# Optimization experiments

Hardware: AMD Instinct MI355X
Metric: run time of the kernel (lower is better)

The kernel has to match this reference:

```python
import jax, jax.numpy as jnp
import numpy as np

EPS = 1e-12


def _gather_neighbors(t, idx):
    # t: (bs, v, d), idx: (bs, v, n) -> (bs, v, n, d)  [torch: t[arange(bs)[:,None,None], idx]]
    bs, v, n = idx.shape
    flat = jnp.take_along_axis(t, idx.reshape(bs, v * n)[..., None], axis=1)
    return flat.reshape(bs, v, n, t.shape[-1])


def setup_inputs() -> dict:
    key = jax.random.key(0)
    ks = jax.random.split(key, 9)
    bs, v, n, inc, outc, sup = 8, 2048, 20, 64, 128, 2
    return {
        "neighbor_index": jax.random.randint(ks[0], (bs, v, n), 0, v),
        "vertices": jax.random.normal(ks[1], (bs, v, 3), dtype=jnp.float32),
        "feature_map": jax.random.normal(ks[2], (bs, v, inc), dtype=jnp.float32),
        "weights": jax.random.normal(ks[3], (inc, (sup + 1) * outc), dtype=jnp.float32) * 0.05,
        "bias": jax.random.normal(ks[4], ((sup + 1) * outc,), dtype=jnp.float32) * 0.05,
        "directions": jax.random.normal(ks[5], (3, sup * outc), dtype=jnp.float32) * 0.05,
        "distance_w": jax.random.normal(ks[6], (1, sup * outc), dtype=jnp.float32) * 0.05,
        "mlp_w": jax.random.normal(ks[7], (outc, 2 * outc), dtype=jnp.float32) * 0.05,
        "mlp_b": jax.random.normal(ks[8], (outc,), dtype=jnp.float32) * 0.05,
    }


def reference(neighbor_index, vertices, feature_map, weights, bias, directions, distance_w, mlp_w, mlp_b):
    bs, v, n = neighbor_index.shape
    outc = mlp_w.shape[0]
    sup = directions.shape[1] // outc

    # neighbor directions and distances (single gather, reuse norm)
    neighbors = _gather_neighbors(vertices, neighbor_index)          # (bs,v,n,3)
    direction = neighbors - vertices[:, :, None, :]                  # (bs,v,n,3)
    dist = jnp.linalg.norm(direction, axis=-1)                       # (bs,v,n)
    dir_norm = direction / jnp.maximum(dist[..., None], EPS)         # F.normalize
    dist_max = jnp.max(dist, axis=2, keepdims=True)                  # (bs,v,1)

    # support directions normalized along dim 0
    sdn = directions / jnp.maximum(jnp.linalg.norm(directions, axis=0, keepdims=True), EPS)
    theta = jax.nn.relu(jnp.einsum('bvnc,cs->bvns', dir_norm, sdn))  # (bs,v,n,sup*outc)
    dist_feat = jax.nn.relu(dist_max @ distance_w)                   # (bs,v,sup*outc)

    feat = feature_map @ weights + bias                              # (bs,v,(sup+1)*outc)
    center = feat[..., :outc]
    support = feat[..., outc:]
    support_g = _gather_neighbors(support, neighbor_index)           # (bs,v,n,sup*outc)

    act = (theta * support_g).reshape(bs, v, n, sup, outc)
    act = jnp.sum(jnp.max(act, axis=2), axis=2)                      # max over neighbors, sum over supports
    fuse = center + act                                              # (bs,v,outc)
    dist_sum = jnp.sum(dist_feat.reshape(bs, v, sup, outc), axis=2)  # (bs,v,outc)

    out = jnp.concatenate([fuse, dist_sum], axis=-1)                 # (bs,v,2*outc)
    return out @ mlp_w.T + mlp_b                                     # (bs,v,outc)
```

## Files before the change

### kernel.cpp

```cpp
#include <hip/hip_runtime.h>
#include <hip/hip_bf16.h>

#define BS    8
#define V     2048
#define NNB   20
#define INC   64
#define OUTC  128
#define SUP   2
#define NCOL  ((SUP + 1) * OUTC)
#define SCOL  (SUP * OUTC)
#define ROWS  (BS * V)
#define XPAD  136

using bf16x8 = __bf16 __attribute__((ext_vector_type(8)));
using bf16x4 = __bf16 __attribute__((ext_vector_type(4)));
using f32x4  = float  __attribute__((ext_vector_type(4)));
using f32x2  = float  __attribute__((ext_vector_type(2)));
using i32x4  = int    __attribute__((ext_vector_type(4)));
using u16x4  = unsigned short __attribute__((ext_vector_type(4)));

#if __has_builtin(__builtin_elementwise_fma)
static __device__ inline f32x2 efma(f32x2 a, f32x2 b, f32x2 c) { return __builtin_elementwise_fma(a, b, c); }
#else
static __device__ inline f32x2 efma(f32x2 a, f32x2 b, f32x2 c) {
    f32x2 r; r[0] = fmaf(a[0], b[0], c[0]); r[1] = fmaf(a[1], b[1], c[1]); return r;
}
#endif
#if __has_builtin(__builtin_elementwise_max)
static __device__ inline f32x2 emax(f32x2 a, f32x2 b) { return __builtin_elementwise_max(a, b); }
#else
static __device__ inline f32x2 emax(f32x2 a, f32x2 b) {
    f32x2 r; r[0] = fmaxf(a[0], b[0]); r[1] = fmaxf(a[1], b[1]); return r;
}
#endif

static __device__ inline bf16x8 cvt8(f32x4 lo, f32x4 hi) {
    bf16x8 r;
    r[0] = (__bf16)lo[0]; r[1] = (__bf16)lo[1]; r[2] = (__bf16)lo[2]; r[3] = (__bf16)lo[3];
    r[4] = (__bf16)hi[0]; r[5] = (__bf16)hi[1]; r[6] = (__bf16)hi[2]; r[7] = (__bf16)hi[3];
    return r;
}

static __device__ inline float b2f(unsigned short u) {
    union { unsigned int i; float f; } c; c.i = ((unsigned int)u) << 16; return c.f;
}

__global__ __launch_bounds__(256) void k_prep(const float* __restrict__ W,
                                              const float* __restrict__ Wm,
                                              const float* __restrict__ dw,
                                              __bf16* __restrict__ WTb,
                                              __bf16* __restrict__ Wm1b,
                                              float* __restrict__ w2) {
    const int b = blockIdx.x;
    if (b < 96) {
        const int idx = b * 256 + threadIdx.x;
        const int c = idx >> 6, k = idx & 63;
        WTb[idx] = (__bf16)W[k * NCOL + c];
    } else if (b < 160) {
        const int idx = (b - 96) * 256 + threadIdx.x;
        const int o = idx >> 7, k = idx & 127;
        Wm1b[idx] = (__bf16)Wm[o * SCOL + k];
    } else {
        __shared__ float u[OUTC];
        const int t = threadIdx.x;
        if (t < OUTC) u[t] = fmaxf(dw[t], 0.f) + fmaxf(dw[OUTC + t], 0.f);
        __syncthreads();
        if (t < OUTC) {
            float s = 0.f;
            for (int k = 0; k < OUTC; ++k) s = fmaf(Wm[t * SCOL + OUTC + k], u[k], s);
            w2[t] = s;
        }
    }
}

__global__ __launch_bounds__(256) void k_feat(const float* __restrict__ fm,
                                              const __bf16* __restrict__ WTb,
                                              const float* __restrict__ bias,
                                              float* __restrict__ center,
                                              __bf16* __restrict__ supb) {
    const int row0 = blockIdx.x * 32;
    const int wid = threadIdx.x >> 6, lane = threadIdx.x & 63;
    const int ln = lane & 15, lg = lane >> 4;
    const int cbase = wid * 96;

    bf16x8 a[2][2];
#pragma unroll
    for (int rs = 0; rs < 2; ++rs) {
        const float* ap = fm + (size_t)(row0 + rs * 16 + ln) * INC + lg * 8;
        a[rs][0] = cvt8(*(const f32x4*)(ap +  0), *(const f32x4*)(ap +  4));
        a[rs][1] = cvt8(*(const f32x4*)(ap + 32), *(const f32x4*)(ap + 36));
    }

    f32x4 acc[2][6];
#pragma unroll
    for (int t = 0; t < 6; ++t) {
        const float bb = bias[cbase + t * 16 + ln];
        acc[0][t] = (f32x4){bb, bb, bb, bb};
        acc[1][t] = acc[0][t];
    }

    const __bf16* bp = WTb + (size_t)(cbase + ln) * INC + lg * 8;
#pragma unroll
    for (int t = 0; t < 6; ++t) {
        const bf16x8 b0 = *(const bf16x8*)(bp + t * 16 * INC);
        const bf16x8 b1 = *(const bf16x8*)(bp + t * 16 * INC + 32);
        acc[0][t] = __builtin_amdgcn_mfma_f32_16x16x32_bf16(a[0][0], b0, acc[0][t], 0, 0, 0);
        acc[0][t] = __builtin_amdgcn_mfma_f32_16x16x32_bf16(a[0][1], b1, acc[0][t], 0, 0, 0);
        acc[1][t] = __builtin_amdgcn_mfma_f32_16x16x32_bf16(a[1][0], b0, acc[1][t], 0, 0, 0);
        acc[1][t] = __builtin_amdgcn_mfma_f32_16x16x32_bf16(a[1][1], b1, acc[1][t], 0, 0, 0);
    }

#pragma unroll
    for (int rs = 0; rs < 2; ++rs) {
        const int r0 = row0 + rs * 16 + lg * 4;
#pragma unroll
        for (int t = 0; t < 6; ++t) {
            const int col = cbase + t * 16 + ln;
            if (col < OUTC) {
#pragma unroll
                for (int r = 0; r < 4; ++r)
                    center[(size_t)(r0 + r) * OUTC + col] = acc[rs][t][r];
            } else {
                const int sc = col - OUTC;
#pragma unroll
                for (int r = 0; r < 4; ++r)
                    supb[(size_t)(r0 + r) * SCOL + sc] = (__bf16)acc[rs][t][r];
            }
        }
    }
}

__global__ __launch_bounds__(256, 4) void k_no(const int*   __restrict__ nbr,
                                               const float* __restrict__ verts,
                                               const float* __restrict__ dirs,
                                               const float* __restrict__ center,
                                               const __bf16* __restrict__ supb,
                                               const __bf16* __restrict__ Wm1b,
                                               const float* __restrict__ w2,
                                               const float* __restrict__ mb,
                                               float* __restrict__ out) {
    const int bid   = blockIdx.x;
    const int batch = bid & 7;
    const int chunk = bid >> 3;
    const int u0    = chunk * 16;
    const int bV    = batch * V;
    const int tid   = threadIdx.x;
    const int wid   = tid >> 6;
    const int lane  = tid & 63;
    const int half  = lane >> 5;
    const int sl    = lane & 31;
    const int c0    = sl * 4;
    const int ln    = lane & 15, lg = lane >> 4;

    __shared__ __bf16 Xl[16][XPAD];
    __shared__ float  dl[16];

    f32x4 A0 = *(const f32x4*)(dirs +            c0);
    f32x4 A1 = *(const f32x4*)(dirs + SCOL +     c0);
    f32x4 A2 = *(const f32x4*)(dirs + 2*SCOL +   c0);
    f32x4 B0 = *(const f32x4*)(dirs +            OUTC + c0);
    f32x4 B1 = *(const f32x4*)(dirs + SCOL +     OUTC + c0);
    f32x4 B2 = *(const f32x4*)(dirs + 2*SCOL +   OUTC + c0);
#pragma unroll
    for (int j = 0; j < 4; ++j) {
        float inv = __builtin_amdgcn_rsqf(fmaxf(fmaf(A0[j], A0[j], fmaf(A1[j], A1[j], A2[j]*A2[j])), 1e-24f));
        A0[j] *= inv; A1[j] *= inv; A2[j] *= inv;
        inv = __builtin_amdgcn_rsqf(fmaxf(fmaf(B0[j], B0[j], fmaf(B1[j], B1[j], B2[j]*B2[j])), 1e-24f));
        B0[j] *= inv; B1[j] *= inv; B2[j] *= inv;
    }
    const f32x2 ax0 = {A0[0], A0[1]}, ax1 = {A0[2], A0[3]};
    const f32x2 ay0 = {A1[0], A1[1]}, ay1 = {A1[2], A1[3]};
    const f32x2 az0 = {A2[0], A2[1]}, az1 = {A2[2], A2[3]};
    const f32x2 bx0 = {B0[0], B0[1]}, bx1 = {B0[2], B0[3]};
    const f32x2 by0 = {B1[0], B1[1]}, by1 = {B1[2], B1[3]};
    const f32x2 bz0 = {B2[0], B2[1]}, bz1 = {B2[2], B2[3]};
    const f32x2 zero = {0.f, 0.f};

    const __bf16* supBase = supb + (size_t)bV * SCOL + c0;

#pragma unroll
    for (int p = 0; p < 2; ++p) {
        const int ul  = p * 8 + wid * 2 + half;
        const int row = bV + u0 + ul;

        const float vx = verts[row * 3 + 0];
        const float vy = verts[row * 3 + 1];
        const float vz = verts[row * 3 + 2];

        int gs[NNB];
        {
            const i32x4* np4 = reinterpret_cast<const i32x4*>(nbr + (size_t)row * NNB);
#pragma unroll
            for (int t = 0; t < 5; ++t) {
                const i32x4 g4 = np4[t];
                gs[t*4+0] = g4[0]; gs[t*4+1] = g4[1]; gs[t*4+2] = g4[2]; gs[t*4+3] = g4[3];
            }
        }

        f32x2 mA0 = {-INFINITY, -INFINITY}, mA1 = mA0, mB0 = mA0, mB1 = mA0;
        float d2max = 0.f;

#pragma unroll
        for (int t = 0; t < 4; ++t) {
            u16x4 s0r[5], s1r[5];
            float px[5], py[5], pz[5];
#pragma unroll
            for (int q = 0; q < 5; ++q) {
                const int g = gs[t * 5 + q];
                const __bf16* sg = supBase + (size_t)g * SCOL;
                s0r[q] = *(const u16x4*)(sg);
                s1r[q] = *(const u16x4*)(sg + OUTC);
                const float* vp = verts + (size_t)(bV + g) * 3;
                px[q] = vp[0]; py[q] = vp[1]; pz[q] = vp[2];
            }
#pragma unroll
            for (int q = 0; q < 5; ++q) {
                const float dx = px[q] - vx, dy = py[q] - vy, dz = pz[q] - vz;
                const float d2 = fmaf(dx, dx, fmaf(dy, dy, dz * dz));
                d2max = fmaxf(d2max, d2);
                const float inv = __builtin_amdgcn_rsqf(fmaxf(d2, 1e-24f));
                const f32x2 nX = {dx * inv, dx * inv};
                const f32x2 nY = {dy * inv, dy * inv};
                const f32x2 nZ = {dz * inv, dz * inv};

                const f32x2 s0lo = {b2f(s0r[q][0]), b2f(s0r[q][1])};
                const f32x2 s0hi = {b2f(s0r[q][2]), b2f(s0r[q][3])};
                const f32x2 s1lo = {b2f(s1r[q][0]), b2f(s1r[q][1])};
                const f32x2 s1hi = {b2f(s1r[q][2]), b2f(s1r[q][3])};

                const f32x2 tA0 = emax(efma(nZ, az0, efma(nY, ay0, nX * ax0)), zero);
                const f32x2 tA1 = emax(efma(nZ, az1, efma(nY, ay1, nX * ax1)), zero);
                const f32x2 tB0 = emax(efma(nZ, bz0, efma(nY, by0, nX * bx0)), zero);
                const f32x2 tB1 = emax(efma(nZ, bz1, efma(nY, by1, nX * bx1)), zero);
                mA0 = emax(mA0, tA0 * s0lo);
                mA1 = emax(mA1, tA1 * s0hi);
                mB0 = emax(mB0, tB0 * s1lo);
                mB1 = emax(mB1, tB1 * s1hi);
            }
        }

        const f32x4 cc = *(const f32x4*)(center + (size_t)row * OUTC + c0);
        const f32x2 f01 = (f32x2){cc[0], cc[1]} + mA0 + mB0;
        const f32x2 f23 = (f32x2){cc[2], cc[3]} + mA1 + mB1;
        bf16x4 fx;
        fx[0] = (__bf16)f01[0]; fx[1] = (__bf16)f01[1];
        fx[2] = (__bf16)f23[0]; fx[3] = (__bf16)f23[1];
        *(bf16x4*)(&Xl[ul][c0]) = fx;
        if (sl == 0) dl[ul] = sqrtf(d2max);
    }
    __syncthreads();

    {
        const int cb = wid * 32;

        bf16x8 a[4];
#pragma unroll
        for (int kf = 0; kf < 4; ++kf)
            a[kf] = *(const bf16x8*)(&Xl[ln][lg * 8 + kf * 32]);

        f32x4 acc[2];
        acc[0] = (f32x4)0.f; acc[1] = (f32x4)0.f;

        const __bf16* bp = Wm1b + (size_t)(cb + ln) * OUTC + lg * 8;
#pragma unroll
        for (int t = 0; t < 2; ++t) {
#pragma unroll
            for (int kf = 0; kf < 4; ++kf) {
                const bf16x8 b = *(const bf16x8*)(bp + t * 16 * OUTC + kf * 32);
                acc[t] = __builtin_amdgcn_mfma_f32_16x16x32_bf16(a[kf], b, acc[t], 0, 0, 0);
            }
        }

        float dm[4];
#pragma unroll
        for (int r = 0; r < 4; ++r) dm[r] = dl[lg * 4 + r];

        const int rowg0 = bV + u0 + lg * 4;
#pragma unroll
        for (int t = 0; t < 2; ++t) {
            const int col = cb + t * 16 + ln;
            const float w2c = w2[col];
            const float bb  = mb[col];
#pragma unroll
            for (int r = 0; r < 4; ++r)
                out[(size_t)(rowg0 + r) * OUTC + col] = fmaf(dm[r], w2c, acc[t][r] + bb);
        }
    }
}

extern "C" void kernel_launch(void* const* d_in, const int* in_sizes, int n_in,
                              void* d_out, int out_size, void* d_ws, size_t ws_size,
                              hipStream_t stream) {
    const int*   nbr   = (const int*)  d_in[0];
    const float* verts = (const float*)d_in[1];
    const float* fm    = (const float*)d_in[2];
    const float* W     = (const float*)d_in[3];
    const float* bias  = (const float*)d_in[4];
    const float* dirs  = (const float*)d_in[5];
    const float* dw    = (const float*)d_in[6];
    const float* Wm    = (const float*)d_in[7];
    const float* mb    = (const float*)d_in[8];
    float* out = (float*)d_out;

    float*  center  = (float*)d_ws;
    __bf16* supb    = (__bf16*)(center + (size_t)ROWS * OUTC);
    __bf16* WTb     = supb + (size_t)ROWS * SCOL;
    __bf16* Wm1b    = WTb + NCOL * INC;
    float*  w2      = (float*)(Wm1b + OUTC * OUTC);

    k_prep <<<161,        256, 0, stream>>>(W, Wm, dw, WTb, Wm1b, w2);
    k_feat <<<ROWS / 32,  256, 0, stream>>>(fm, WTb, bias, center, supb);
    k_no   <<<ROWS / 16,  256, 0, stream>>>(nbr, verts, dirs, center, supb, Wm1b, w2, mb, out);
}
```

Measured before the change: 117.3 us.

## Interleave vertex coordinates into support rows and halve rows per block

Packs each vertex's xyz into a padded slot at the end of its bf16 support-feature row, so a neighbor gather gets features and coordinates from one contiguous row rather than from two arrays. k_prep gains blocks that write the coordinates, and the gather loop is regrouped as 5x4 instead of 4x5. k_no now handles 8 vertices per block with twice as many blocks and an occupancy hint of 8. The MFMA tail still computes 16 rows, so half of that work is discarded.

```diff
diff --git a/kernel.cpp b/kernel.cpp
--- a/kernel.cpp
+++ b/kernel.cpp
@@ -12,6 +12,10 @@
 #define ROWS  (BS * V)
 #define XPAD  136
 
+#define SROW_B   528
+#define SROW_E   264
+#define XYZ_OFF  512
+
 using bf16x8 = __bf16 __attribute__((ext_vector_type(8)));
 using bf16x4 = __bf16 __attribute__((ext_vector_type(4)));
 using f32x4  = float  __attribute__((ext_vector_type(4)));
@@ -48,9 +52,11 @@
 __global__ __launch_bounds__(256) void k_prep(const float* __restrict__ W,
                                               const float* __restrict__ Wm,
                                               const float* __restrict__ dw,
+                                              const float* __restrict__ verts,
                                               __bf16* __restrict__ WTb,
                                               __bf16* __restrict__ Wm1b,
-                                              float* __restrict__ w2) {
+                                              float* __restrict__ w2,
+                                              __bf16* __restrict__ supx) {
     const int b = blockIdx.x;
     if (b < 96) {
         const int idx = b * 256 + threadIdx.x;
@@ -60,7 +66,7 @@
         const int idx = (b - 96) * 256 + threadIdx.x;
         const int o = idx >> 7, k = idx & 127;
         Wm1b[idx] = (__bf16)Wm[o * SCOL + k];
-    } else {
+    } else if (b == 160) {
         __shared__ float u[OUTC];
         const int t = threadIdx.x;
         if (t < OUTC) u[t] = fmaxf(dw[t], 0.f) + fmaxf(dw[OUTC + t], 0.f);
@@ -70,6 +76,14 @@
             for (int k = 0; k < OUTC; ++k) s = fmaf(Wm[t * SCOL + OUTC + k], u[k], s);
             w2[t] = s;
         }
+    } else {
+        const int idx = (b - 161) * 256 + threadIdx.x;
+        f32x4 wv;
+        wv[0] = verts[(size_t)idx * 3 + 0];
+        wv[1] = verts[(size_t)idx * 3 + 1];
+        wv[2] = verts[(size_t)idx * 3 + 2];
+        wv[3] = 0.f;
+        *(f32x4*)((char*)supx + (size_t)idx * SROW_B + XYZ_OFF) = wv;
     }
 }
 
@@ -77,7 +91,7 @@
                                               const __bf16* __restrict__ WTb,
                                               const float* __restrict__ bias,
                                               float* __restrict__ center,
-                                              __bf16* __restrict__ supb) {
+                                              __bf16* __restrict__ supx) {
     const int row0 = blockIdx.x * 32;
     const int wid = threadIdx.x >> 6, lane = threadIdx.x & 63;
     const int ln = lane & 15, lg = lane >> 4;
@@ -124,17 +138,16 @@
                 const int sc = col - OUTC;
 #pragma unroll
                 for (int r = 0; r < 4; ++r)
-                    supb[(size_t)(r0 + r) * SCOL + sc] = (__bf16)acc[rs][t][r];
-            }
-        }
-    }
-}
-
-__global__ __launch_bounds__(256, 4) void k_no(const int*   __restrict__ nbr,
-                                               const float* __restrict__ verts,
+                    supx[(size_t)(r0 + r) * SROW_E + sc] = (__bf16)acc[rs][t][r];
+            }
+        }
+    }
+}
+
+__global__ __launch_bounds__(256, 8) void k_no(const int*   __restrict__ nbr,
                                                const float* __restrict__ dirs,
                                                const float* __restrict__ center,
-                                               const __bf16* __restrict__ supb,
+                                               const __bf16* __restrict__ supx,
                                                const __bf16* __restrict__ Wm1b,
                                                const float* __restrict__ w2,
                                                const float* __restrict__ mb,
@@ -142,7 +155,7 @@
     const int bid   = blockIdx.x;
     const int batch = bid & 7;
     const int chunk = bid >> 3;
-    const int u0    = chunk * 16;
+    const int u0    = chunk * 8;
     const int bV    = batch * V;
     const int tid   = threadIdx.x;
     const int wid   = tid >> 6;
@@ -176,16 +189,15 @@
     const f32x2 bz0 = {B2[0], B2[1]}, bz1 = {B2[2], B2[3]};
     const f32x2 zero = {0.f, 0.f};
 
-    const __bf16* supBase = supb + (size_t)bV * SCOL + c0;
-
-#pragma unroll
-    for (int p = 0; p < 2; ++p) {
-        const int ul  = p * 8 + wid * 2 + half;
-        const int row = bV + u0 + ul;
-
-        const float vx = verts[row * 3 + 0];
-        const float vy = verts[row * 3 + 1];
-        const float vz = verts[row * 3 + 2];
+    const char* supB = (const char*)supx + (size_t)bV * SROW_B;
+
+    {
+        const int ul  = wid * 2 + half;
+        const int u   = u0 + ul;
+        const int row = bV + u;
+
+        const f32x4 self = *(const f32x4*)(supB + (size_t)u * SROW_B + XYZ_OFF);
+        const float vx = self[0], vy = self[1], vz = self[2];
 
         int gs[NNB];
         {
@@ -201,21 +213,19 @@
         float d2max = 0.f;
 
 #pragma unroll
-        for (int t = 0; t < 4; ++t) {
-            u16x4 s0r[5], s1r[5];
-            float px[5], py[5], pz[5];
-#pragma unroll
-            for (int q = 0; q < 5; ++q) {
-                const int g = gs[t * 5 + q];
-                const __bf16* sg = supBase + (size_t)g * SCOL;
-                s0r[q] = *(const u16x4*)(sg);
-                s1r[q] = *(const u16x4*)(sg + OUTC);
-                const float* vp = verts + (size_t)(bV + g) * 3;
-                px[q] = vp[0]; py[q] = vp[1]; pz[q] = vp[2];
-            }
-#pragma unroll
-            for (int q = 0; q < 5; ++q) {
-                const float dx = px[q] - vx, dy = py[q] - vy, dz = pz[q] - vz;
+        for (int t = 0; t < 5; ++t) {
+            u16x4 s0r[4], s1r[4];
+            f32x4 nxyz[4];
+#pragma unroll
+            for (int q = 0; q < 4; ++q) {
+                const char* nb = supB + (size_t)gs[t * 4 + q] * SROW_B + (size_t)(sl * 8);
+                s0r[q]  = *(const u16x4*)(nb);
+                s1r[q]  = *(const u16x4*)(nb + 256);
+                nxyz[q] = *(const f32x4*)(supB + (size_t)gs[t * 4 + q] * SROW_B + XYZ_OFF);
+            }
+#pragma unroll
+            for (int q = 0; q < 4; ++q) {
+                const float dx = nxyz[q][0] - vx, dy = nxyz[q][1] - vy, dz = nxyz[q][2] - vz;
                 const float d2 = fmaf(dx, dx, fmaf(dy, dy, dz * dz));
                 d2max = fmaxf(d2max, d2);
                 const float inv = __builtin_amdgcn_rsqf(fmaxf(d2, 1e-24f));
@@ -271,19 +281,21 @@
             }
         }
 
-        float dm[4];
-#pragma unroll
-        for (int r = 0; r < 4; ++r) dm[r] = dl[lg * 4 + r];
-
-        const int rowg0 = bV + u0 + lg * 4;
-#pragma unroll
-        for (int t = 0; t < 2; ++t) {
-            const int col = cb + t * 16 + ln;
-            const float w2c = w2[col];
-            const float bb  = mb[col];
-#pragma unroll
-            for (int r = 0; r < 4; ++r)
-                out[(size_t)(rowg0 + r) * OUTC + col] = fmaf(dm[r], w2c, acc[t][r] + bb);
+        if (lg < 2) {
+            float dm[4];
+#pragma unroll
+            for (int r = 0; r < 4; ++r) dm[r] = dl[lg * 4 + r];
+
+            const int rowg0 = bV + u0 + lg * 4;
+#pragma unroll
+            for (int t = 0; t < 2; ++t) {
+                const int col = cb + t * 16 + ln;
+                const float w2c = w2[col];
+                const float bb  = mb[col];
+#pragma unroll
+                for (int r = 0; r < 4; ++r)
+                    out[(size_t)(rowg0 + r) * OUTC + col] = fmaf(dm[r], w2c, acc[t][r] + bb);
+            }
         }
     }
 }
@@ -303,12 +315,12 @@
     float* out = (float*)d_out;
 
     float*  center  = (float*)d_ws;
-    __bf16* supb    = (__bf16*)(center + (size_t)ROWS * OUTC);
-    __bf16* WTb     = supb + (size_t)ROWS * SCOL;
+    __bf16* supx    = (__bf16*)(center + (size_t)ROWS * OUTC);
+    __bf16* WTb     = supx + (size_t)ROWS * SROW_E;
     __bf16* Wm1b    = WTb + NCOL * INC;
     float*  w2      = (float*)(Wm1b + OUTC * OUTC);
 
-    k_prep <<<161,        256, 0, stream>>>(W, Wm, dw, WTb, Wm1b, w2);
-    k_feat <<<ROWS / 32,  256, 0, stream>>>(fm, WTb, bias, center, supb);
-    k_no   <<<ROWS / 16,  256, 0, stream>>>(nbr, verts, dirs, center, supb, Wm1b, w2, mb, out);
-}
+    k_prep <<<225,        256, 0, stream>>>(W, Wm, dw, verts, WTb, Wm1b, w2, supx);
+    k_feat <<<ROWS / 32,  256, 0, stream>>>(fm, WTb, bias, center, supx);
+    k_no   <<<ROWS / 8,   256, 0, stream>>>(nbr, dirs, center, supx, Wm1b, w2, mb, out);
+}
```

Measured after the change: 243.8 us. 108% more time.
